# Performance work log

Measured on AMD Instinct MI355X. Metric: run time of the kernel, lower is better.

## Reference

```python
import jax, jax.numpy as jnp
import numpy as np

FWD_W = 1.0
BWD_W = 1.0
EPS = 1e-12  # guard sqrt gradient at exact zero


def setup_inputs() -> dict:
    key = jax.random.key(0)
    k1, k2 = jax.random.split(key)
    pred = jax.random.normal(k1, (4, 8192, 3), dtype=jnp.float32)
    target = jax.random.normal(k2, (4, 8192, 3), dtype=jnp.float32)
    return {"pred": pred, "target": target}


def reference(pred, target):
    # pairwise Euclidean distances (torch.cdist, p=2): (B, N, M)
    sq = (jnp.sum(pred * pred, axis=-1)[:, :, None]
          + jnp.sum(target * target, axis=-1)[:, None, :]
          - 2.0 * jnp.einsum('bnd,bmd->bnm', pred, target))
    dist = jnp.sqrt(jnp.maximum(sq, EPS))
    forward_dist = jnp.min(dist, axis=2)   # (B, N): pred -> nearest target
    backward_dist = jnp.min(dist, axis=1)  # (B, M): target -> nearest pred
    total = FWD_W * jnp.sum(forward_dist, axis=1) + BWD_W * jnp.sum(backward_dist, axis=1)
    return jnp.mean(total)  # reduction='mean'
```

## Files before the change

### kernel.cpp

```cpp
#include <hip/hip_runtime.h>
#include <math.h>

#define BATCH   4
#define NPTS    8192
#define THREADS 256
#define CHUNK   1024
#define NCHUNKS (NPTS / CHUNK)
#define NBLOCKS (2 * BATCH * (NPTS / 128))

typedef _Float16 h8   __attribute__((ext_vector_type(8)));
typedef float    f16v __attribute__((ext_vector_type(16)));

__global__ __launch_bounds__(THREADS, 2)
void chamfer_fused_kernel(const float* __restrict__ pred,
                          const float* __restrict__ target,
                          float* __restrict__ bsum)
{
    __shared__ uint4 slo[CHUNK];
    __shared__ uint4 shi[CHUNK];
    __shared__ float sqq[128];
    __shared__ float wsum[8];

    const int tid  = threadIdx.x;
    const int lane = tid & 63;
    const int wave = tid >> 6;
    const int n    = lane & 31;
    const int hi   = lane >> 5;

    const int bid = blockIdx.x;
    const int qg  = bid & 63;
    const int b   = (bid >> 6) & 3;
    const int dir = bid >> 8;

    const float* qraw = ((dir == 0) ? pred : target) + (size_t)b * NPTS * 3;
    const float* draw = ((dir == 0) ? target : pred) + (size_t)b * NPTS * 3;

    const int qtbase = qg * 128 + wave * 32;

    h8 afrag;
    {
        const float* qp = qraw + (size_t)(qtbase + n) * 3;
        const float x = qp[0], y = qp[1], z = qp[2];
        const _Float16 hx = (_Float16)x; const _Float16 lx = (_Float16)(x - (float)hx);
        const _Float16 hy = (_Float16)y; const _Float16 ly = (_Float16)(y - (float)hy);
        const _Float16 hz = (_Float16)z; const _Float16 lz = (_Float16)(z - (float)hz);
        const _Float16 one  = (_Float16)1.0f;
        const _Float16 zero = (_Float16)0.0f;
        if (hi == 0) {
            afrag = (h8){hx, hy, hz, one, lx, ly, lz, one};
            sqq[wave * 32 + n] = fmaf(x, x, fmaf(y, y, z * z));
        } else {
            afrag = (h8){hx, hy, hz, zero, zero, zero, zero, zero};
        }
    }

    float mn[16];
    #pragma unroll
    for (int i = 0; i < 16; ++i) mn[i] = 3.0e38f;

    const float4* dra4 = (const float4*)draw;
    const uint4*  bsrc = hi ? shi : slo;

    for (int c = 0; c < NCHUNKS; ++c) {
        {
            const int base4 = c * 768 + 3 * tid;
            const float4 f0 = dra4[base4 + 0];
            const float4 f1 = dra4[base4 + 1];
            const float4 f2 = dra4[base4 + 2];
            const float px[4] = {f0.x, f0.w, f1.z, f2.y};
            const float py[4] = {f0.y, f1.x, f1.w, f2.z};
            const float pz[4] = {f0.z, f1.y, f2.x, f2.w};

            #pragma unroll
            for (int k = 0; k < 4; ++k) {
                const float x = px[k], y = py[k], z = pz[k];
                const _Float16 hx = (_Float16)x; const _Float16 lx = (_Float16)(x - (float)hx);
                const _Float16 hy = (_Float16)y; const _Float16 ly = (_Float16)(y - (float)hy);
                const _Float16 hz = (_Float16)z; const _Float16 lz = (_Float16)(z - (float)hz);
                const float tx = (float)hx + (float)lx;
                const float ty = (float)hy + (float)ly;
                const float tz = (float)hz + (float)lz;
                const float tt = fmaf(tx, tx, fmaf(ty, ty, tz * tz));
                const _Float16 tth = (_Float16)tt;
                const _Float16 ttl = (_Float16)(tt - (float)tth);
                const _Float16 n2 = (_Float16)(-2.0f);
                const _Float16 zz = (_Float16)0.0f;
                h8 lo = { n2 * hx, n2 * hy, n2 * hz, tth,
                          n2 * hx, n2 * hy, n2 * hz, ttl };
                h8 hh = { n2 * lx, n2 * ly, n2 * lz, zz, zz, zz, zz, zz };
                const int slot = 4 * tid + k;
                slo[slot] = *(const uint4*)&lo;
                shi[slot] = *(const uint4*)&hh;
            }
        }
        __syncthreads();

        #pragma unroll 2
        for (int t = 0; t < CHUNK / 32; ++t) {
            const h8 bfrag = *(const h8*)&bsrc[t * 32 + n];
            const f16v zc = {};
            const f16v d = __builtin_amdgcn_mfma_f32_32x32x16_f16(afrag, bfrag, zc, 0, 0, 0);
            #pragma unroll
            for (int i = 0; i < 16; ++i)
                mn[i] = fminf(mn[i], d[i]);
        }
        __syncthreads();
    }

    #pragma unroll
    for (int mask = 1; mask <= 16; mask <<= 1) {
        #pragma unroll
        for (int i = 0; i < 16; ++i)
            mn[i] = fminf(mn[i], __shfl_xor(mn[i], mask, 64));
    }

    if (n == 0) {
        float s = 0.0f;
        #pragma unroll
        for (int i = 0; i < 16; ++i) {
            const int row = (i & 3) + 8 * (i >> 2) + 4 * hi;
            s += sqrtf(fmaxf(sqq[wave * 32 + row] + mn[i], 1e-12f));
        }
        wsum[wave * 2 + hi] = s;
    }
    __syncthreads();
    if (tid == 0) {
        float t = 0.0f;
        #pragma unroll
        for (int k = 0; k < 8; ++k) t += wsum[k];
        bsum[bid] = t;
    }
}

__global__ __launch_bounds__(THREADS)
void chamfer_final(const float* __restrict__ bsum,
                   float* __restrict__ out)
{
    const int tid = threadIdx.x;
    float v = bsum[tid] + bsum[tid + 256];
    #pragma unroll
    for (int off = 32; off > 0; off >>= 1)
        v += __shfl_down(v, off, 64);

    __shared__ float wsum[4];
    if ((tid & 63) == 0) wsum[tid >> 6] = v;
    __syncthreads();
    if (tid == 0) out[0] = (wsum[0] + wsum[1] + wsum[2] + wsum[3]) * (1.0f / BATCH);
}

extern "C" void kernel_launch(void* const* d_in, const int* in_sizes, int n_in,
                              void* d_out, int out_size, void* d_ws, size_t ws_size,
                              hipStream_t stream)
{
    const float* pred   = (const float*)d_in[0];
    const float* target = (const float*)d_in[1];
    float* out          = (float*)d_out;
    float* bsum         = (float*)d_ws;

    chamfer_fused_kernel<<<NBLOCKS, THREADS, 0, stream>>>(pred, target, bsum);
    chamfer_final<<<1, THREADS, 0, stream>>>(bsum, out);
}
```

Measured before the change: 85.99 us.

## Precompute split-fp16 target fragments in a separate kernel and software-pipeline MFMA loop

Moves the per-point fp16 hi/lo split and norm computation out of the main kernel into a prepass that writes packed fragments to workspace, so each of the 512 blocks copies them into LDS instead of recomputing the conversion. The inner MFMA loop is restructured to issue four MFMAs per iteration, with the next fragments prefetched from LDS before the min-reduction. The occupancy hint on launch bounds is also dropped. This adds a kernel launch and extra global traffic (2 MB of fragments read repeatedly) in exchange for removing redundant conversion ALU work.

```diff
diff --git a/kernel.cpp b/kernel.cpp
--- a/kernel.cpp
+++ b/kernel.cpp
@@ -11,10 +11,46 @@
 typedef _Float16 h8   __attribute__((ext_vector_type(8)));
 typedef float    f16v __attribute__((ext_vector_type(16)));
 
-__global__ __launch_bounds__(THREADS, 2)
-void chamfer_fused_kernel(const float* __restrict__ pred,
-                          const float* __restrict__ target,
-                          float* __restrict__ bsum)
+__global__ __launch_bounds__(THREADS)
+void chamfer_transform(const float* __restrict__ pred,
+                       const float* __restrict__ target,
+                       h8* __restrict__ trans_lo,
+                       h8* __restrict__ trans_hi)
+{
+    const int p   = blockIdx.x * THREADS + threadIdx.x;
+    const int arr = p >> 15;
+    const int pb  = p & 32767;
+
+    const float* src = (arr ? target : pred) + (size_t)pb * 3;
+    const float x = src[0], y = src[1], z = src[2];
+
+    const _Float16 hx = (_Float16)x;  const _Float16 lx = (_Float16)(x - (float)hx);
+    const _Float16 hy = (_Float16)y;  const _Float16 ly = (_Float16)(y - (float)hy);
+    const _Float16 hz = (_Float16)z;  const _Float16 lz = (_Float16)(z - (float)hz);
+
+    const float tx = (float)hx + (float)lx;
+    const float ty = (float)hy + (float)ly;
+    const float tz = (float)hz + (float)lz;
+    const float tt = fmaf(tx, tx, fmaf(ty, ty, tz * tz));
+    const _Float16 tth = (_Float16)tt;
+    const _Float16 ttl = (_Float16)(tt - (float)tth);
+
+    const _Float16 n2 = (_Float16)(-2.0f);
+    const _Float16 zz = (_Float16)0.0f;
+    h8 lo = { n2 * hx, n2 * hy, n2 * hz, tth,
+              n2 * hx, n2 * hy, n2 * hz, ttl };
+    h8 hi = { n2 * lx, n2 * ly, n2 * lz, zz, zz, zz, zz, zz };
+
+    trans_lo[p] = lo;
+    trans_hi[p] = hi;
+}
+
+__global__ __launch_bounds__(THREADS)
+void chamfer_min_kernel(const float* __restrict__ pred,
+                        const float* __restrict__ target,
+                        const uint4* __restrict__ trans_lo,
+                        const uint4* __restrict__ trans_hi,
+                        float* __restrict__ bsum)
 {
     __shared__ uint4 slo[CHUNK];
     __shared__ uint4 shi[CHUNK];
@@ -33,9 +69,8 @@
     const int dir = bid >> 8;
 
     const float* qraw = ((dir == 0) ? pred : target) + (size_t)b * NPTS * 3;
-    const float* draw = ((dir == 0) ? target : pred) + (size_t)b * NPTS * 3;
-
-    const int qtbase = qg * 128 + wave * 32;
+    const int    darr = (dir == 0) ? 1 : 0;
+    const int    qtbase = qg * 128 + wave * 32;
 
     h8 afrag;
     {
@@ -58,51 +93,41 @@
     #pragma unroll
     for (int i = 0; i < 16; ++i) mn[i] = 3.0e38f;
 
-    const float4* dra4 = (const float4*)draw;
-    const uint4*  bsrc = hi ? shi : slo;
+    const f16v zc = {};
+    const uint4* bsrc = hi ? shi : slo;
+    const size_t gbase = (size_t)(darr * 4 + b) * NPTS;
 
+    #pragma unroll 1
     for (int c = 0; c < NCHUNKS; ++c) {
-        {
-            const int base4 = c * 768 + 3 * tid;
-            const float4 f0 = dra4[base4 + 0];
-            const float4 f1 = dra4[base4 + 1];
-            const float4 f2 = dra4[base4 + 2];
-            const float px[4] = {f0.x, f0.w, f1.z, f2.y};
-            const float py[4] = {f0.y, f1.x, f1.w, f2.z};
-            const float pz[4] = {f0.z, f1.y, f2.x, f2.w};
-
-            #pragma unroll
-            for (int k = 0; k < 4; ++k) {
-                const float x = px[k], y = py[k], z = pz[k];
-                const _Float16 hx = (_Float16)x; const _Float16 lx = (_Float16)(x - (float)hx);
-                const _Float16 hy = (_Float16)y; const _Float16 ly = (_Float16)(y - (float)hy);
-                const _Float16 hz = (_Float16)z; const _Float16 lz = (_Float16)(z - (float)hz);
-                const float tx = (float)hx + (float)lx;
-                const float ty = (float)hy + (float)ly;
-                const float tz = (float)hz + (float)lz;
-                const float tt = fmaf(tx, tx, fmaf(ty, ty, tz * tz));
-                const _Float16 tth = (_Float16)tt;
-                const _Float16 ttl = (_Float16)(tt - (float)tth);
-                const _Float16 n2 = (_Float16)(-2.0f);
-                const _Float16 zz = (_Float16)0.0f;
-                h8 lo = { n2 * hx, n2 * hy, n2 * hz, tth,
-                          n2 * hx, n2 * hy, n2 * hz, ttl };
-                h8 hh = { n2 * lx, n2 * ly, n2 * lz, zz, zz, zz, zz, zz };
-                const int slot = 4 * tid + k;
-                slo[slot] = *(const uint4*)&lo;
-                shi[slot] = *(const uint4*)&hh;
-            }
+        const size_t cb = gbase + (size_t)c * CHUNK;
+        #pragma unroll
+        for (int r = 0; r < 4; ++r) {
+            slo[r * THREADS + tid] = trans_lo[cb + r * THREADS + tid];
+            shi[r * THREADS + tid] = trans_hi[cb + r * THREADS + tid];
         }
         __syncthreads();
 
-        #pragma unroll 2
-        for (int t = 0; t < CHUNK / 32; ++t) {
-            const h8 bfrag = *(const h8*)&bsrc[t * 32 + n];
-            const f16v zc = {};
-            const f16v d = __builtin_amdgcn_mfma_f32_32x32x16_f16(afrag, bfrag, zc, 0, 0, 0);
+        h8 bf0 = *(const h8*)&bsrc[0 * 32 + n];
+        h8 bf1 = *(const h8*)&bsrc[1 * 32 + n];
+        h8 bf2 = *(const h8*)&bsrc[2 * 32 + n];
+        h8 bf3 = *(const h8*)&bsrc[3 * 32 + n];
+
+        #pragma unroll 1
+        for (int t = 0; t < 32; t += 4) {
+            const f16v d0 = __builtin_amdgcn_mfma_f32_32x32x16_f16(afrag, bf0, zc, 0, 0, 0);
+            const f16v d1 = __builtin_amdgcn_mfma_f32_32x32x16_f16(afrag, bf1, zc, 0, 0, 0);
+            const f16v d2 = __builtin_amdgcn_mfma_f32_32x32x16_f16(afrag, bf2, zc, 0, 0, 0);
+            const f16v d3 = __builtin_amdgcn_mfma_f32_32x32x16_f16(afrag, bf3, zc, 0, 0, 0);
+
+            const int tn = (t + 4) & 31;
+            bf0 = *(const h8*)&bsrc[(tn + 0) * 32 + n];
+            bf1 = *(const h8*)&bsrc[(tn + 1) * 32 + n];
+            bf2 = *(const h8*)&bsrc[(tn + 2) * 32 + n];
+            bf3 = *(const h8*)&bsrc[(tn + 3) * 32 + n];
+
             #pragma unroll
             for (int i = 0; i < 16; ++i)
-                mn[i] = fminf(mn[i], d[i]);
+                mn[i] = fminf(fminf(fminf(fminf(mn[i], d0[i]), d1[i]), d2[i]), d3[i]);
         }
         __syncthreads();
     }
@@ -155,8 +180,13 @@
     const float* pred   = (const float*)d_in[0];
     const float* target = (const float*)d_in[1];
     float* out          = (float*)d_out;
-    float* bsum         = (float*)d_ws;
 
-    chamfer_fused_kernel<<<NBLOCKS, THREADS, 0, stream>>>(pred, target, bsum);
+    h8*    trans_lo = (h8*)d_ws;
+    h8*    trans_hi = (h8*)((char*)d_ws + (size_t)65536 * 16);
+    float* bsum     = (float*)((char*)d_ws + (size_t)131072 * 16);
+
+    chamfer_transform<<<256, THREADS, 0, stream>>>(pred, target, trans_lo, trans_hi);
+    chamfer_min_kernel<<<NBLOCKS, THREADS, 0, stream>>>(
+        pred, target, (const uint4*)trans_lo, (const uint4*)trans_hi, bsum);
     chamfer_final<<<1, THREADS, 0, stream>>>(bsum, out);
 }
```

New measurement: 91.27 us. 1.06x slower.
